# Optimization experiments

Measured on AMD Instinct MI355X. Metric: run time of the kernel, lower is better.

Reference implementation:

```python
import jax, jax.numpy as jnp
import numpy as np
from jax import lax

N, CI, CO, H, W = 2, 256, 256, 64, 64
K, G, DIL, PAD, STRIDE = 3, 8, 1, 1, 1
P = K * K
CG = CO // G  # group channels = 32


def setup_inputs() -> dict:
    key = jax.random.key(0)
    ks = jax.random.split(key, 24)
    r = lambda i, shape, s=1.0: jax.random.normal(ks[i], shape, jnp.float32) * s
    u = lambda i, shape: jax.random.uniform(ks[i], shape, jnp.float32, 0.5, 1.5)
    return dict(
        x=r(0, (N, CI, H, W)),
        conv1_w=r(1, (CO, CI), CI ** -0.5),
        bn1_g=u(2, (CO,)), bn1_b=r(3, (CO,), 0.1), bn1_m=r(4, (CO,), 0.1), bn1_v=u(5, (CO,)),
        inproj_w=r(6, (CO, CO), CO ** -0.5), inproj_b=r(7, (CO,), 0.02),
        dw_w=r(8, (CO, 1, K, K), 0.2), dw_b=r(9, (CO,), 0.02),
        ln_g=u(10, (CO,)), ln_b=r(11, (CO,), 0.02),
        off_w=r(12, (CO, G * P * 2), CO ** -0.5), off_b=jnp.zeros((G * P * 2,), jnp.float32),
        mask_w=r(13, (CO, G * P), CO ** -0.5), mask_b=jnp.zeros((G * P,), jnp.float32),
        outproj_w=r(14, (CO, CO), CO ** -0.5), outproj_b=r(15, (CO,), 0.02),
        bn2_g=u(16, (CO,)), bn2_b=r(17, (CO,), 0.1), bn2_m=r(18, (CO,), 0.1), bn2_v=u(19, (CO,)),
    )


def _bn(x, g, b, m, v, eps):
    # inference-mode BatchNorm2d on NCHW
    return (x - m[:, None, None]) * (g[:, None, None] * lax.rsqrt(v[:, None, None] + eps)) + b[:, None, None]


def _dcn_core(t, offset, mask):
    # t: (N,H,W,C) projected input; offset: (N,H,W,G*P*2); mask: (N,H,W,G,P) softmaxed
    xp = jnp.pad(t, ((0, 0), (PAD, PAD), (PAD, PAD), (0, 0)))
    H_, W_ = H + 2 * PAD, W + 2 * PAD
    # reference points (sample centers), normalized to padded size
    ry = ((DIL * (K - 1)) / 2 + 0.5 + STRIDE * jnp.arange(H, dtype=t.dtype)) / H_
    rx = ((DIL * (K - 1)) / 2 + 0.5 + STRIDE * jnp.arange(W, dtype=t.dtype)) / W_
    base = (DIL * (K - 1)) // 2
    gx = jnp.linspace(-base, -base + (K - 1) * DIL, K, dtype=t.dtype) / W_
    gy = jnp.linspace(-base, -base + (K - 1) * DIL, K, dtype=t.dtype) / H_
    gxx, gyy = jnp.meshgrid(gx, gy, indexing='ij')  # x varies along axis 0 (torch meshgrid order)
    grid = jnp.stack([gxx, gyy], -1).reshape(P, 2)  # (P,2)
    off = offset.reshape(N, H, W, G, P, 2) / jnp.array([W_, H_], t.dtype)
    loc_x = rx[None, None, :, None, None] + grid[:, 0][None, None, None, None] + off[..., 0]  # (N,H,W,G,P)
    loc_y = ry[None, :, None, None, None] + grid[:, 1][None, None, None, None] + off[..., 1]
    # grid_sample(align_corners=False): pixel = norm*size - 0.5
    px = jnp.transpose(loc_x * W_ - 0.5, (0, 3, 1, 2, 4)).reshape(N, G, H * W * P)
    py = jnp.transpose(loc_y * H_ - 0.5, (0, 3, 1, 2, 4)).reshape(N, G, H * W * P)
    # grouped channels-last image: (N,G,H_*W_,CG)
    xg = jnp.transpose(xp.reshape(N, H_, W_, G, CG), (0, 3, 1, 2, 4)).reshape(N, G, H_ * W_, CG)
    x0 = jnp.floor(px)
    y0 = jnp.floor(py)
    wx1 = px - x0
    wy1 = py - y0
    x0i = x0.astype(jnp.int32)
    y0i = y0.astype(jnp.int32)

    def corner(xi, yi, w):
        valid = (xi >= 0) & (xi <= W_ - 1) & (yi >= 0) & (yi <= H_ - 1)
        idx = jnp.clip(yi, 0, H_ - 1) * W_ + jnp.clip(xi, 0, W_ - 1)
        v = jnp.take_along_axis(xg, idx[..., None], axis=2)  # (N,G,M,CG)
        return v * jnp.where(valid, w, 0.0)[..., None]

    sampled = (corner(x0i, y0i, (1 - wx1) * (1 - wy1))
               + corner(x0i + 1, y0i, wx1 * (1 - wy1))
               + corner(x0i, y0i + 1, (1 - wx1) * wy1)
               + corner(x0i + 1, y0i + 1, wx1 * wy1))
    sampled = sampled.reshape(N, G, H * W, P, CG)
    mg = jnp.transpose(mask, (0, 3, 1, 2, 4)).reshape(N, G, H * W, P)
    out = jnp.einsum('nglpc,nglp->nglc', sampled, mg)
    return jnp.transpose(out, (0, 2, 1, 3)).reshape(N, H, W, G * CG)


def reference(x, conv1_w, bn1_g, bn1_b, bn1_m, bn1_v, inproj_w, inproj_b, dw_w, dw_b,
              ln_g, ln_b, off_w, off_b, mask_w, mask_b, outproj_w, outproj_b,
              bn2_g, bn2_b, bn2_m, bn2_v):
    # Conv(inc, ouc, k=1): 1x1 conv (no bias) + BN(eps=1e-3) + SiLU
    y = jnp.einsum('nchw,oc->nohw', x, conv1_w)
    y = jax.nn.silu(_bn(y, bn1_g, bn1_b, bn1_m, bn1_v, 1e-3))
    t = jnp.transpose(y, (0, 2, 3, 1))  # NHWC
    xproj = t @ inproj_w + inproj_b     # input_proj Linear
    # offset/mask branch: depthwise conv (k=3,s=1,p=1) -> LN over C -> GELU
    z = lax.conv_general_dilated(y, dw_w, (1, 1), ((PAD, PAD), (PAD, PAD)),
                                 feature_group_count=CO,
                                 dimension_numbers=('NCHW', 'OIHW', 'NCHW')) + dw_b[None, :, None, None]
    z = jnp.transpose(z, (0, 2, 3, 1))
    mu = jnp.mean(z, -1, keepdims=True)
    var = jnp.var(z, -1, keepdims=True)
    z = (z - mu) * lax.rsqrt(var + 1e-5) * ln_g + ln_b
    z = jax.nn.gelu(z, approximate=False)
    offset = z @ off_w + off_b  # (N,H,W,G*P*2)
    mask = jax.nn.softmax((z @ mask_w + mask_b).reshape(N, H, W, G, P), axis=-1)
    s = _dcn_core(xproj, offset, mask)
    s = s @ outproj_w + outproj_b  # output_proj Linear
    o = jnp.transpose(s, (0, 3, 1, 2))  # back to NCHW
    return jax.nn.silu(_bn(o, bn2_g, bn2_b, bn2_m, bn2_v, 1e-5))
```

## Files before the change

kernel.cpp:

```cpp
#include <hip/hip_runtime.h>
#include <math.h>

#define CC    256
#define HH    64
#define WW    64
#define HWSZ  4096
#define NPIX  8192
#define MT    16
#define TT    8
#define ASTR  264

typedef __attribute__((ext_vector_type(8))) short short8;
typedef __attribute__((ext_vector_type(4))) float f32x4;

__device__ __forceinline__ float silu_f(float x) { return x / (1.f + __expf(-x)); }

__device__ __forceinline__ short f2bf(float f) {
    unsigned u = __float_as_uint(f);
    unsigned r = (u + 0x7fffu + ((u >> 16) & 1u)) >> 16;
    return (short)r;
}
__device__ __forceinline__ unsigned pk2(float a, float b) {
    return (unsigned)(unsigned short)f2bf(a) | ((unsigned)(unsigned short)f2bf(b) << 16);
}
__device__ __forceinline__ float4 bf4(uint2 u) {
    float4 r;
    r.x = __uint_as_float(u.x << 16);
    r.y = __uint_as_float(u.x & 0xffff0000u);
    r.z = __uint_as_float(u.y << 16);
    r.w = __uint_as_float(u.y & 0xffff0000u);
    return r;
}

__global__ void k_prep(const float* __restrict__ cw, const float* __restrict__ ipw,
                       const float* __restrict__ offw, const float* __restrict__ maskw,
                       const float* __restrict__ opw,
                       const float* __restrict__ offb, const float* __restrict__ maskb,
                       const float* __restrict__ g1, const float* __restrict__ b1,
                       const float* __restrict__ m1, const float* __restrict__ v1,
                       const float* __restrict__ g2, const float* __restrict__ b2,
                       const float* __restrict__ m2, const float* __restrict__ v2,
                       short* __restrict__ Wc1b, short* __restrict__ Wipb,
                       short* __restrict__ Whb, short* __restrict__ Wopb,
                       float* __restrict__ bh, float* __restrict__ sc1, float* __restrict__ sh1,
                       float* __restrict__ sc2, float* __restrict__ sh2) {
    int o = blockIdx.x, c = threadIdx.x;
    Wc1b[o * CC + c] = f2bf(cw[o * CC + c]);
    Wipb[o * CC + c] = f2bf(ipw[c * CC + o]);
    float hv = 0.f;
    if (o < 144) hv = offw[c * 144 + o];
    else if (o < 216) hv = maskw[c * 72 + (o - 144)];
    Whb[o * CC + c] = f2bf(hv);
    Wopb[o * CC + c] = f2bf(opw[c * CC + o]);
    if (o == 0) {
        float bv = 0.f;
        if (c < 144) bv = offb[c];
        else if (c < 216) bv = maskb[c - 144];
        bh[c] = bv;
        float s1 = g1[c] * rsqrtf(v1[c] + 1e-3f);
        sc1[c] = s1; sh1[c] = b1[c] - m1[c] * s1;
        float s2 = g2[c] * rsqrtf(v2[c] + 1e-5f);
        sc2[c] = s2; sh2[c] = b2[c] - m2[c] * s2;
    }
}

__device__ __forceinline__ void gemm2(const short* As, const short* __restrict__ Wb,
                                      int lane, int n0, f32x4 acc[2]) {
    const int m = lane & 15, q = lane >> 4;
#pragma unroll
    for (int kk = 0; kk < 8; ++kk) {
        int c0 = kk * 32 + q * 8;
        short8 a = *(const short8*)(As + m * ASTR + c0);
#pragma unroll
        for (int nt = 0; nt < 2; ++nt) {
            short8 b = *(const short8*)(Wb + (size_t)(n0 + nt * 16 + m) * CC + c0);
            acc[nt] = __builtin_amdgcn_mfma_f32_16x16x32_bf16(a, b, acc[nt], 0, 0, 0);
        }
    }
}

__global__ __launch_bounds__(512, 4) void k_conv_in(
        const float* __restrict__ x, const short* __restrict__ Wc1b,
        const short* __restrict__ Wipb, const float* __restrict__ sc1,
        const float* __restrict__ sh1, const float* __restrict__ ipb,
        float* __restrict__ y, short* __restrict__ xpb) {
    __shared__ __align__(16) short As[MT * ASTR];
    int tid = threadIdx.x, lane = tid & 63, wv = tid >> 6;
    int pix0 = blockIdx.x * MT;
    int n = pix0 >> 12, hw0 = pix0 & (HWSZ - 1);
    int n0 = wv * 32;
    const float* xn = x + (size_t)n * CC * HWSZ;
#pragma unroll
    for (int rep = 0; rep < 2; ++rep) {
        int f = tid + rep * 512;
        int c = f >> 2, i4 = (f & 3) * 4;
        float4 v = *(const float4*)(xn + (size_t)c * HWSZ + hw0 + i4);
        As[(i4 + 0) * ASTR + c] = f2bf(v.x);
        As[(i4 + 1) * ASTR + c] = f2bf(v.y);
        As[(i4 + 2) * ASTR + c] = f2bf(v.z);
        As[(i4 + 3) * ASTR + c] = f2bf(v.w);
    }
    __syncthreads();
    f32x4 acc[2];
    acc[0] = (f32x4){0.f, 0.f, 0.f, 0.f};
    acc[1] = (f32x4){0.f, 0.f, 0.f, 0.f};
    gemm2(As, Wc1b, lane, n0, acc);
    __syncthreads();
    int col = lane & 15, qr = (lane >> 4) * 4;
#pragma unroll
    for (int nt = 0; nt < 2; ++nt) {
        int o = n0 + nt * 16 + col;
        float sc = sc1[o], sh = sh1[o];
#pragma unroll
        for (int r = 0; r < 4; ++r) {
            int pix = qr + r;
            float val = silu_f(acc[nt][r] * sc + sh);
            y[(size_t)(pix0 + pix) * CC + o] = val;
            As[pix * ASTR + o] = f2bf(val);
        }
    }
    __syncthreads();
    acc[0] = (f32x4){0.f, 0.f, 0.f, 0.f};
    acc[1] = (f32x4){0.f, 0.f, 0.f, 0.f};
    gemm2(As, Wipb, lane, n0, acc);
#pragma unroll
    for (int nt = 0; nt < 2; ++nt) {
        int o = n0 + nt * 16 + col;
        float bo = ipb[o];
#pragma unroll
        for (int r = 0; r < 4; ++r)
            xpb[(size_t)(pix0 + qr + r) * CC + o] = f2bf(acc[nt][r] + bo);
    }
}

__global__ __launch_bounds__(512, 6) void k_tail(
        const float* __restrict__ y, const short* __restrict__ xpb,
        const float* __restrict__ dww, const float* __restrict__ dwb,
        const float* __restrict__ lng, const float* __restrict__ lnb,
        const short* __restrict__ Whb, const float* __restrict__ bh,
        const short* __restrict__ Wopb, const float* __restrict__ opb,
        const float* __restrict__ sc2, const float* __restrict__ sh2,
        float* __restrict__ out) {
    __shared__ __align__(16) short As[16 * ASTR];
    __shared__ float loff[TT * 144];
    __shared__ float ml[TT * 76];

    int tid = threadIdx.x, lane = tid & 63, wv = tid >> 6;
    int pix0 = blockIdx.x * TT;
    int n = pix0 >> 12, hw0 = pix0 & (HWSZ - 1);
    int h = hw0 >> 6, w0 = hw0 & 63;
    int c0 = lane * 4;
    int n0 = wv * 32;
    int col = lane & 15, qr = (lane >> 4) * 4;

    {
        float wloc[36];
        const float4* wp4 = (const float4*)(dww + c0 * 9);
#pragma unroll
        for (int k = 0; k < 9; ++k) ((float4*)wloc)[k] = wp4[k];
        float4 acc = *(const float4*)(dwb + c0);
        float4 lngv = *(const float4*)(lng + c0);
        float4 lnbv = *(const float4*)(lnb + c0);
        const float* yn = y + (size_t)n * HWSZ * CC;
        int w = w0 + wv;
#pragma unroll
        for (int ky = 0; ky < 3; ++ky) {
            int yy = h + ky - 1;
            int yc = min(max(yy, 0), HH - 1);
            float vy = (yy == yc) ? 1.f : 0.f;
#pragma unroll
            for (int kx = 0; kx < 3; ++kx) {
                int xx = w + kx - 1;
                int xc = min(max(xx, 0), WW - 1);
                float vm = vy * ((xx == xc) ? 1.f : 0.f);
                float4 yv = *(const float4*)(yn + (size_t)((yc << 6) + xc) * CC + c0);
                int t = ky * 3 + kx;
                acc.x += yv.x * wloc[0 * 9 + t] * vm;
                acc.y += yv.y * wloc[1 * 9 + t] * vm;
                acc.z += yv.z * wloc[2 * 9 + t] * vm;
                acc.w += yv.w * wloc[3 * 9 + t] * vm;
            }
        }
        float s1 = acc.x + acc.y + acc.z + acc.w;
        float s2 = acc.x * acc.x + acc.y * acc.y + acc.z * acc.z + acc.w * acc.w;
#pragma unroll
        for (int off = 32; off > 0; off >>= 1) {
            s1 += __shfl_xor(s1, off);
            s2 += __shfl_xor(s2, off);
        }
        float mu = s1 * (1.f / 256.f);
        float var = s2 * (1.f / 256.f) - mu * mu;
        float rs = rsqrtf(var + 1e-5f);
        float4 zv;
        zv.x = (acc.x - mu) * rs * lngv.x + lnbv.x;
        zv.y = (acc.y - mu) * rs * lngv.y + lnbv.y;
        zv.z = (acc.z - mu) * rs * lngv.z + lnbv.z;
        zv.w = (acc.w - mu) * rs * lngv.w + lnbv.w;
        zv.x = 0.5f * zv.x * (1.f + erff(zv.x * 0.70710678118654752f));
        zv.y = 0.5f * zv.y * (1.f + erff(zv.y * 0.70710678118654752f));
        zv.z = 0.5f * zv.z * (1.f + erff(zv.z * 0.70710678118654752f));
        zv.w = 0.5f * zv.w * (1.f + erff(zv.w * 0.70710678118654752f));
        *(uint2*)(As + wv * ASTR + c0) = make_uint2(pk2(zv.x, zv.y), pk2(zv.z, zv.w));
    }
    __syncthreads();

    {
        f32x4 acc[2];
        acc[0] = (f32x4){0.f, 0.f, 0.f, 0.f};
        acc[1] = (f32x4){0.f, 0.f, 0.f, 0.f};
        gemm2(As, Whb, lane, n0, acc);
        if (qr < TT) {
#pragma unroll
            for (int nt = 0; nt < 2; ++nt) {
                int o = n0 + nt * 16 + col;
                float bo = bh[o];
#pragma unroll
                for (int r = 0; r < 4; ++r) {
                    float v = acc[nt][r] + bo;
                    int pix = qr + r;
                    if (o < 144) loff[pix * 144 + o] = v;
                    else if (o < 216) ml[pix * 76 + (o - 144)] = v;
                }
            }
        }
    }
    __syncthreads();

    {
        int g = lane >> 3;
        const short* xpn = xpb + (size_t)n * HWSZ * CC;
        int pix = wv;
        int w = w0 + pix;
        float e9[9];
        {
            const float* row = ml + pix * 76 + g * 9;
            float mx = -1e30f;
#pragma unroll
            for (int p = 0; p < 9; ++p) { e9[p] = row[p]; mx = fmaxf(mx, e9[p]); }
            float ssum = 0.f;
#pragma unroll
            for (int p = 0; p < 9; ++p) { e9[p] = __expf(e9[p] - mx); ssum += e9[p]; }
            float inv = 1.f / ssum;
#pragma unroll
            for (int p = 0; p < 9; ++p) e9[p] *= inv;
        }
        const float* lp = loff + pix * 144 + g * 18;
        float4 acc = make_float4(0.f, 0.f, 0.f, 0.f);
#pragma unroll
        for (int p = 0; p < 9; ++p) {
            float ox = lp[p * 2], oy = lp[p * 2 + 1];
            float px = (float)(w + p / 3) + ox;
            float py = (float)(h + p % 3) + oy;
            float fx = floorf(px), fy = floorf(py);
            float wx1 = px - fx, wy1 = py - fy;
            int x0 = (int)fx, y0 = (int)fy;
            int x1 = x0 + 1, y1 = y0 + 1;
            int xc0 = min(max(x0, 1), WW), xc1 = min(max(x1, 1), WW);
            int yc0 = min(max(y0, 1), HH), yc1 = min(max(y1, 1), HH);
            float vx0 = (x0 == xc0) ? 1.f : 0.f, vx1 = (x1 == xc1) ? 1.f : 0.f;
            float vy0 = (y0 == yc0) ? 1.f : 0.f, vy1 = (y1 == yc1) ? 1.f : 0.f;
            float mval = e9[p];
            float w00 = (1.f - wx1) * (1.f - wy1) * mval * vx0 * vy0;
            float w10 = wx1 * (1.f - wy1) * mval * vx1 * vy0;
            float w01 = (1.f - wx1) * wy1 * mval * vx0 * vy1;
            float w11 = wx1 * wy1 * mval * vx1 * vy1;
            uint2 u00 = *(const uint2*)(xpn + (size_t)(((yc0 - 1) << 6) + (xc0 - 1)) * CC + c0);
            uint2 u10 = *(const uint2*)(xpn + (size_t)(((yc0 - 1) << 6) + (xc1 - 1)) * CC + c0);
            uint2 u01 = *(const uint2*)(xpn + (size_t)(((yc1 - 1) << 6) + (xc0 - 1)) * CC + c0);
            uint2 u11 = *(const uint2*)(xpn + (size_t)(((yc1 - 1) << 6) + (xc1 - 1)) * CC + c0);
            float4 s00 = bf4(u00), s10 = bf4(u10), s01 = bf4(u01), s11 = bf4(u11);
            acc.x += w00 * s00.x + w10 * s10.x + w01 * s01.x + w11 * s11.x;
            acc.y += w00 * s00.y + w10 * s10.y + w01 * s01.y + w11 * s11.y;
            acc.z += w00 * s00.z + w10 * s10.z + w01 * s01.z + w11 * s11.z;
            acc.w += w00 * s00.w + w10 * s10.w + w01 * s01.w + w11 * s11.w;
        }
        *(uint2*)(As + pix * ASTR + c0) = make_uint2(pk2(acc.x, acc.y), pk2(acc.z, acc.w));
    }
    __syncthreads();

    {
        f32x4 acc[2];
        acc[0] = (f32x4){0.f, 0.f, 0.f, 0.f};
        acc[1] = (f32x4){0.f, 0.f, 0.f, 0.f};
        gemm2(As, Wopb, lane, n0, acc);
        if (qr < TT) {
            float* ob = out + (size_t)n * CC * HWSZ + hw0 + qr;
#pragma unroll
            for (int nt = 0; nt < 2; ++nt) {
                int o = n0 + nt * 16 + col;
                float bo = opb[o], sc = sc2[o], sh = sh2[o];
                float4 ov;
                ov.x = silu_f((acc[nt][0] + bo) * sc + sh);
                ov.y = silu_f((acc[nt][1] + bo) * sc + sh);
                ov.z = silu_f((acc[nt][2] + bo) * sc + sh);
                ov.w = silu_f((acc[nt][3] + bo) * sc + sh);
                *(float4*)(ob + (size_t)o * HWSZ) = ov;
            }
        }
    }
}

extern "C" void kernel_launch(void* const* d_in, const int* in_sizes, int n_in,
                              void* d_out, int out_size, void* d_ws, size_t ws_size,
                              hipStream_t stream) {
    const float* x        = (const float*)d_in[0];
    const float* conv1_w  = (const float*)d_in[1];
    const float* bn1_g    = (const float*)d_in[2];
    const float* bn1_b    = (const float*)d_in[3];
    const float* bn1_m    = (const float*)d_in[4];
    const float* bn1_v    = (const float*)d_in[5];
    const float* inproj_w = (const float*)d_in[6];
    const float* inproj_b = (const float*)d_in[7];
    const float* dw_w     = (const float*)d_in[8];
    const float* dw_b     = (const float*)d_in[9];
    const float* ln_g     = (const float*)d_in[10];
    const float* ln_b     = (const float*)d_in[11];
    const float* off_w    = (const float*)d_in[12];
    const float* off_b    = (const float*)d_in[13];
    const float* mask_w   = (const float*)d_in[14];
    const float* mask_b   = (const float*)d_in[15];
    const float* outproj_w = (const float*)d_in[16];
    const float* outproj_b = (const float*)d_in[17];
    const float* bn2_g    = (const float*)d_in[18];
    const float* bn2_b    = (const float*)d_in[19];
    const float* bn2_m    = (const float*)d_in[20];
    const float* bn2_v    = (const float*)d_in[21];
    float* out = (float*)d_out;

    short* Wc1b = (short*)d_ws;
    short* Wipb = Wc1b + 65536;
    short* Whb  = Wipb + 65536;
    short* Wopb = Whb + 65536;
    float* fp   = (float*)(Wopb + 65536);
    float* bh   = fp;
    float* sc1  = bh + 256;
    float* sh1  = sc1 + 256;
    float* sc2  = sh1 + 256;
    float* sh2  = sc2 + 256;
    float* y    = sh2 + 256;
    short* xpb  = (short*)(y + 2097152);

    k_prep<<<dim3(CC), dim3(CC), 0, stream>>>(conv1_w, inproj_w, off_w, mask_w, outproj_w,
                                              off_b, mask_b, bn1_g, bn1_b, bn1_m, bn1_v,
                                              bn2_g, bn2_b, bn2_m, bn2_v,
                                              Wc1b, Wipb, Whb, Wopb, bh, sc1, sh1, sc2, sh2);
    k_conv_in<<<dim3(NPIX / MT), dim3(512), 0, stream>>>(x, Wc1b, Wipb, sc1, sh1, inproj_b, y, xpb);
    k_tail<<<dim3(NPIX / TT), dim3(512), 0, stream>>>(y, xpb, dw_w, dw_b, ln_g, ln_b,
                                                      Whb, bh, Wopb, outproj_b, sc2, sh2, out);
}
```

Before: 177.2 us.

## Store conv output in bf16, widen tail tile, vectorize gathers and coalesce output

The intermediate activation y is now stored as bf16 instead of fp32, which halves the traffic for writing it and for reading it back in the depthwise conv. The tail kernel processes 16 pixels per block instead of 8, so the MFMA tiles are fully used and the weight loads are amortised over more pixels. Deformable sampling now uses 16-byte gathers covering 8 channels per lane with two pixels per wave. The output is staged through shared memory so the NCHW stores become coalesced float4 writes. The bf16 y adds rounding error in the depthwise/LN branch, and the larger shared footprint may lower occupancy.

```diff
diff --git a/kernel.cpp b/kernel.cpp
--- a/kernel.cpp
+++ b/kernel.cpp
@@ -7,7 +7,7 @@
 #define HWSZ  4096
 #define NPIX  8192
 #define MT    16
-#define TT    8
+#define TT    16
 #define ASTR  264
 
 typedef __attribute__((ext_vector_type(8))) short short8;
@@ -30,6 +30,16 @@
     r.z = __uint_as_float(u.y << 16);
     r.w = __uint_as_float(u.y & 0xffff0000u);
     return r;
+}
+__device__ __forceinline__ void bf8acc(uint4 u, float wgt, float* acc) {
+    acc[0] += wgt * __uint_as_float(u.x << 16);
+    acc[1] += wgt * __uint_as_float(u.x & 0xffff0000u);
+    acc[2] += wgt * __uint_as_float(u.y << 16);
+    acc[3] += wgt * __uint_as_float(u.y & 0xffff0000u);
+    acc[4] += wgt * __uint_as_float(u.z << 16);
+    acc[5] += wgt * __uint_as_float(u.z & 0xffff0000u);
+    acc[6] += wgt * __uint_as_float(u.w << 16);
+    acc[7] += wgt * __uint_as_float(u.w & 0xffff0000u);
 }
 
 __global__ void k_prep(const float* __restrict__ cw, const float* __restrict__ ipw,
@@ -83,7 +93,7 @@
         const float* __restrict__ x, const short* __restrict__ Wc1b,
         const short* __restrict__ Wipb, const float* __restrict__ sc1,
         const float* __restrict__ sh1, const float* __restrict__ ipb,
-        float* __restrict__ y, short* __restrict__ xpb) {
+        short* __restrict__ ybf, short* __restrict__ xpb) {
     __shared__ __align__(16) short As[MT * ASTR];
     int tid = threadIdx.x, lane = tid & 63, wv = tid >> 6;
     int pix0 = blockIdx.x * MT;
@@ -114,9 +124,9 @@
 #pragma unroll
         for (int r = 0; r < 4; ++r) {
             int pix = qr + r;
-            float val = silu_f(acc[nt][r] * sc + sh);
-            y[(size_t)(pix0 + pix) * CC + o] = val;
-            As[pix * ASTR + o] = f2bf(val);
+            short vb = f2bf(silu_f(acc[nt][r] * sc + sh));
+            ybf[(size_t)(pix0 + pix) * CC + o] = vb;
+            As[pix * ASTR + o] = vb;
         }
     }
     __syncthreads();
@@ -134,16 +144,18 @@
 }
 
 __global__ __launch_bounds__(512, 6) void k_tail(
-        const float* __restrict__ y, const short* __restrict__ xpb,
+        const short* __restrict__ ybf, const short* __restrict__ xpb,
         const float* __restrict__ dww, const float* __restrict__ dwb,
         const float* __restrict__ lng, const float* __restrict__ lnb,
         const short* __restrict__ Whb, const float* __restrict__ bh,
         const short* __restrict__ Wopb, const float* __restrict__ opb,
         const float* __restrict__ sc2, const float* __restrict__ sh2,
         float* __restrict__ out) {
-    __shared__ __align__(16) short As[16 * ASTR];
-    __shared__ float loff[TT * 144];
-    __shared__ float ml[TT * 76];
+    __shared__ __align__(16) short As[TT * ASTR];
+    __shared__ __align__(16) float buf[TT * 260];
+    float* ml   = buf;
+    float* loff = buf + 1216;
+    float* xs   = buf;
 
     int tid = threadIdx.x, lane = tid & 63, wv = tid >> 6;
     int pix0 = blockIdx.x * TT;
@@ -158,49 +170,54 @@
         const float4* wp4 = (const float4*)(dww + c0 * 9);
 #pragma unroll
         for (int k = 0; k < 9; ++k) ((float4*)wloc)[k] = wp4[k];
-        float4 acc = *(const float4*)(dwb + c0);
+        float4 dwbv = *(const float4*)(dwb + c0);
         float4 lngv = *(const float4*)(lng + c0);
         float4 lnbv = *(const float4*)(lnb + c0);
-        const float* yn = y + (size_t)n * HWSZ * CC;
-        int w = w0 + wv;
-#pragma unroll
-        for (int ky = 0; ky < 3; ++ky) {
-            int yy = h + ky - 1;
-            int yc = min(max(yy, 0), HH - 1);
-            float vy = (yy == yc) ? 1.f : 0.f;
-#pragma unroll
-            for (int kx = 0; kx < 3; ++kx) {
-                int xx = w + kx - 1;
-                int xc = min(max(xx, 0), WW - 1);
-                float vm = vy * ((xx == xc) ? 1.f : 0.f);
-                float4 yv = *(const float4*)(yn + (size_t)((yc << 6) + xc) * CC + c0);
-                int t = ky * 3 + kx;
-                acc.x += yv.x * wloc[0 * 9 + t] * vm;
-                acc.y += yv.y * wloc[1 * 9 + t] * vm;
-                acc.z += yv.z * wloc[2 * 9 + t] * vm;
-                acc.w += yv.w * wloc[3 * 9 + t] * vm;
+        const short* yn = ybf + (size_t)n * HWSZ * CC;
+#pragma unroll
+        for (int i = 0; i < 2; ++i) {
+            int pix = wv * 2 + i;
+            int w = w0 + pix;
+            float4 acc = dwbv;
+#pragma unroll
+            for (int ky = 0; ky < 3; ++ky) {
+                int yy = h + ky - 1;
+                int yc = min(max(yy, 0), HH - 1);
+                float vy = (yy == yc) ? 1.f : 0.f;
+#pragma unroll
+                for (int kx = 0; kx < 3; ++kx) {
+                    int xx = w + kx - 1;
+                    int xc = min(max(xx, 0), WW - 1);
+                    float vm = vy * ((xx == xc) ? 1.f : 0.f);
+                    float4 yv = bf4(*(const uint2*)(yn + (size_t)((yc << 6) + xc) * CC + c0));
+                    int t = ky * 3 + kx;
+                    acc.x += yv.x * wloc[0 * 9 + t] * vm;
+                    acc.y += yv.y * wloc[1 * 9 + t] * vm;
+                    acc.z += yv.z * wloc[2 * 9 + t] * vm;
+                    acc.w += yv.w * wloc[3 * 9 + t] * vm;
+                }
             }
-        }
-        float s1 = acc.x + acc.y + acc.z + acc.w;
-        float s2 = acc.x * acc.x + acc.y * acc.y + acc.z * acc.z + acc.w * acc.w;
-#pragma unroll
-        for (int off = 32; off > 0; off >>= 1) {
-            s1 += __shfl_xor(s1, off);
-            s2 += __shfl_xor(s2, off);
-        }
-        float mu = s1 * (1.f / 256.f);
-        float var = s2 * (1.f / 256.f) - mu * mu;
-        float rs = rsqrtf(var + 1e-5f);
-        float4 zv;
-        zv.x = (acc.x - mu) * rs * lngv.x + lnbv.x;
-        zv.y = (acc.y - mu) * rs * lngv.y + lnbv.y;
-        zv.z = (acc.z - mu) * rs * lngv.z + lnbv.z;
-        zv.w = (acc.w - mu) * rs * lngv.w + lnbv.w;
-        zv.x = 0.5f * zv.x * (1.f + erff(zv.x * 0.70710678118654752f));
-        zv.y = 0.5f * zv.y * (1.f + erff(zv.y * 0.70710678118654752f));
-        zv.z = 0.5f * zv.z * (1.f + erff(zv.z * 0.70710678118654752f));
-        zv.w = 0.5f * zv.w * (1.f + erff(zv.w * 0.70710678118654752f));
-        *(uint2*)(As + wv * ASTR + c0) = make_uint2(pk2(zv.x, zv.y), pk2(zv.z, zv.w));
+            float s1 = acc.x + acc.y + acc.z + acc.w;
+            float s2 = acc.x * acc.x + acc.y * acc.y + acc.z * acc.z + acc.w * acc.w;
+#pragma unroll
+            for (int off = 32; off > 0; off >>= 1) {
+                s1 += __shfl_xor(s1, off);
+                s2 += __shfl_xor(s2, off);
+            }
+            float mu = s1 * (1.f / 256.f);
+            float var = s2 * (1.f / 256.f) - mu * mu;
+            float rs = rsqrtf(var + 1e-5f);
+            float4 zv;
+            zv.x = (acc.x - mu) * rs * lngv.x + lnbv.x;
+            zv.y = (acc.y - mu) * rs * lngv.y + lnbv.y;
+            zv.z = (acc.z - mu) * rs * lngv.z + lnbv.z;
+            zv.w = (acc.w - mu) * rs * lngv.w + lnbv.w;
+            zv.x = 0.5f * zv.x * (1.f + erff(zv.x * 0.70710678118654752f));
+            zv.y = 0.5f * zv.y * (1.f + erff(zv.y * 0.70710678118654752f));
+            zv.z = 0.5f * zv.z * (1.f + erff(zv.z * 0.70710678118654752f));
+            zv.w = 0.5f * zv.w * (1.f + erff(zv.w * 0.70710678118654752f));
+            *(uint2*)(As + pix * ASTR + c0) = make_uint2(pk2(zv.x, zv.y), pk2(zv.z, zv.w));
+        }
     }
     __syncthreads();
 
@@ -209,27 +226,27 @@
         acc[0] = (f32x4){0.f, 0.f, 0.f, 0.f};
         acc[1] = (f32x4){0.f, 0.f, 0.f, 0.f};
         gemm2(As, Whb, lane, n0, acc);
-        if (qr < TT) {
-#pragma unroll
-            for (int nt = 0; nt < 2; ++nt) {
-                int o = n0 + nt * 16 + col;
-                float bo = bh[o];
-#pragma unroll
-                for (int r = 0; r < 4; ++r) {
-                    float v = acc[nt][r] + bo;
-                    int pix = qr + r;
-                    if (o < 144) loff[pix * 144 + o] = v;
-                    else if (o < 216) ml[pix * 76 + (o - 144)] = v;
-                }
+#pragma unroll
+        for (int nt = 0; nt < 2; ++nt) {
+            int o = n0 + nt * 16 + col;
+            float bo = bh[o];
+#pragma unroll
+            for (int r = 0; r < 4; ++r) {
+                float v = acc[nt][r] + bo;
+                int pix = qr + r;
+                if (o < 144) loff[pix * 144 + o] = v;
+                else if (o < 216) ml[pix * 76 + (o - 144)] = v;
             }
         }
     }
     __syncthreads();
 
     {
-        int g = lane >> 3;
-        const short* xpn = xpb + (size_t)n * HWSZ * CC;
-        int pix = wv;
+        int ph = lane >> 5;
+        int g  = (lane >> 2) & 7;
+        int ci = lane & 3;
+        int gc0 = g * 32 + ci * 8;
+        int pix = wv * 2 + ph;
         int w = w0 + pix;
         float e9[9];
         {
@@ -245,7 +262,10 @@
             for (int p = 0; p < 9; ++p) e9[p] *= inv;
         }
         const float* lp = loff + pix * 144 + g * 18;
-        float4 acc = make_float4(0.f, 0.f, 0.f, 0.f);
+        const short* xpn = xpb + (size_t)n * HWSZ * CC;
+        float acc8[8];
+#pragma unroll
+        for (int k = 0; k < 8; ++k) acc8[k] = 0.f;
 #pragma unroll
         for (int p = 0; p < 9; ++p) {
             float ox = lp[p * 2], oy = lp[p * 2 + 1];
@@ -264,17 +284,21 @@
             float w10 = wx1 * (1.f - wy1) * mval * vx1 * vy0;
             float w01 = (1.f - wx1) * wy1 * mval * vx0 * vy1;
             float w11 = wx1 * wy1 * mval * vx1 * vy1;
-            uint2 u00 = *(const uint2*)(xpn + (size_t)(((yc0 - 1) << 6) + (xc0 - 1)) * CC + c0);
-            uint2 u10 = *(const uint2*)(xpn + (size_t)(((yc0 - 1) << 6) + (xc1 - 1)) * CC + c0);
-            uint2 u01 = *(const uint2*)(xpn + (size_t)(((yc1 - 1) << 6) + (xc0 - 1)) * CC + c0);
-            uint2 u11 = *(const uint2*)(xpn + (size_t)(((yc1 - 1) << 6) + (xc1 - 1)) * CC + c0);
-            float4 s00 = bf4(u00), s10 = bf4(u10), s01 = bf4(u01), s11 = bf4(u11);
-            acc.x += w00 * s00.x + w10 * s10.x + w01 * s01.x + w11 * s11.x;
-            acc.y += w00 * s00.y + w10 * s10.y + w01 * s01.y + w11 * s11.y;
-            acc.z += w00 * s00.z + w10 * s10.z + w01 * s01.z + w11 * s11.z;
-            acc.w += w00 * s00.w + w10 * s10.w + w01 * s01.w + w11 * s11.w;
-        }
-        *(uint2*)(As + pix * ASTR + c0) = make_uint2(pk2(acc.x, acc.y), pk2(acc.z, acc.w));
+            uint4 u00 = *(const uint4*)(xpn + (size_t)(((yc0 - 1) << 6) + (xc0 - 1)) * CC + gc0);
+            uint4 u10 = *(const uint4*)(xpn + (size_t)(((yc0 - 1) << 6) + (xc1 - 1)) * CC + gc0);
+            uint4 u01 = *(const uint4*)(xpn + (size_t)(((yc1 - 1) << 6) + (xc0 - 1)) * CC + gc0);
+            uint4 u11 = *(const uint4*)(xpn + (size_t)(((yc1 - 1) << 6) + (xc1 - 1)) * CC + gc0);
+            bf8acc(u00, w00, acc8);
+            bf8acc(u10, w10, acc8);
+            bf8acc(u01, w01, acc8);
+            bf8acc(u11, w11, acc8);
+        }
+        uint4 pkv;
+        pkv.x = pk2(acc8[0], acc8[1]);
+        pkv.y = pk2(acc8[2], acc8[3]);
+        pkv.z = pk2(acc8[4], acc8[5]);
+        pkv.w = pk2(acc8[6], acc8[7]);
+        *(uint4*)(As + pix * ASTR + gc0) = pkv;
     }
     __syncthreads();
 
@@ -283,19 +307,31 @@
         acc[0] = (f32x4){0.f, 0.f, 0.f, 0.f};
         acc[1] = (f32x4){0.f, 0.f, 0.f, 0.f};
         gemm2(As, Wopb, lane, n0, acc);
-        if (qr < TT) {
-            float* ob = out + (size_t)n * CC * HWSZ + hw0 + qr;
-#pragma unroll
-            for (int nt = 0; nt < 2; ++nt) {
-                int o = n0 + nt * 16 + col;
-                float bo = opb[o], sc = sc2[o], sh = sh2[o];
-                float4 ov;
-                ov.x = silu_f((acc[nt][0] + bo) * sc + sh);
-                ov.y = silu_f((acc[nt][1] + bo) * sc + sh);
-                ov.z = silu_f((acc[nt][2] + bo) * sc + sh);
-                ov.w = silu_f((acc[nt][3] + bo) * sc + sh);
-                *(float4*)(ob + (size_t)o * HWSZ) = ov;
-            }
+        __syncthreads();
+#pragma unroll
+        for (int nt = 0; nt < 2; ++nt) {
+            int o = n0 + nt * 16 + col;
+            float bo = opb[o], sc = sc2[o], sh = sh2[o];
+#pragma unroll
+            for (int r = 0; r < 4; ++r)
+                xs[(qr + r) * 260 + o] = silu_f((acc[nt][r] + bo) * sc + sh);
+        }
+    }
+    __syncthreads();
+
+    {
+        int i4 = (tid & 3) * 4;
+        int obase = tid >> 2;
+        float* on = out + (size_t)n * CC * HWSZ + hw0 + i4;
+#pragma unroll
+        for (int pass = 0; pass < 2; ++pass) {
+            int o = obase + pass * 128;
+            float4 ov;
+            ov.x = xs[(i4 + 0) * 260 + o];
+            ov.y = xs[(i4 + 1) * 260 + o];
+            ov.z = xs[(i4 + 2) * 260 + o];
+            ov.w = xs[(i4 + 3) * 260 + o];
+            *(float4*)(on + (size_t)o * HWSZ) = ov;
         }
     }
 }
@@ -337,14 +373,14 @@
     float* sh1  = sc1 + 256;
     float* sc2  = sh1 + 256;
     float* sh2  = sc2 + 256;
-    float* y    = sh2 + 256;
-    short* xpb  = (short*)(y + 2097152);
+    short* ybf  = (short*)(sh2 + 256);
+    short* xpb  = ybf + (size_t)NPIX * CC;
 
     k_prep<<<dim3(CC), dim3(CC), 0, stream>>>(conv1_w, inproj_w, off_w, mask_w, outproj_w,
                                               off_b, mask_b, bn1_g, bn1_b, bn1_m, bn1_v,
                                               bn2_g, bn2_b, bn2_m, bn2_v,
                                               Wc1b, Wipb, Whb, Wopb, bh, sc1, sh1, sc2, sh2);
-    k_conv_in<<<dim3(NPIX / MT), dim3(512), 0, stream>>>(x, Wc1b, Wipb, sc1, sh1, inproj_b, y, xpb);
-    k_tail<<<dim3(NPIX / TT), dim3(512), 0, stream>>>(y, xpb, dw_w, dw_b, ln_g, ln_b,
+    k_conv_in<<<dim3(NPIX / MT), dim3(512), 0, stream>>>(x, Wc1b, Wipb, sc1, sh1, inproj_b, ybf, xpb);
+    k_tail<<<dim3(NPIX / TT), dim3(512), 0, stream>>>(ybf, xpb, dw_w, dw_b, ln_g, ln_b,
                                                       Whb, bh, Wopb, outproj_b, sc2, sh2, out);
 }
```

Measured after the change: 178.3 us. About the same (+0.6%).
